# Kernel optimization log

Measured on AMD Instinct MI355X. Metric: run time of the kernel, lower is better.

## Reference

```python
import jax, jax.numpy as jnp
from jax import lax
import numpy as np

LRELU_SLOPE = 0.2
DEMOD_EPS = 1e-8


def _mod_conv(x, style, weight, bias, demodulate, pad):
    """StyleGAN2 modulated conv via grouped conv (groups = batch).
    x: [B,Cin,H,W]; style: [B,Cin]; weight: [Cout,Cin,kh,kw]; bias: [Cout]."""
    B, Cin, H, W = x.shape
    Cout, _, kh, kw = weight.shape
    # per-sample modulated weight [B,Cout,Cin,kh,kw]
    wt = weight[None] * style[:, None, :, None, None]
    if demodulate:
        wt = wt / jnp.sqrt(jnp.sum(wt ** 2, axis=(2, 3, 4), keepdims=True) + DEMOD_EPS)
    out = lax.conv_general_dilated(
        x.reshape(1, B * Cin, H, W),
        wt.reshape(B * Cout, Cin, kh, kw),
        window_strides=(1, 1),
        padding=[(pad, pad), (pad, pad)],
        dimension_numbers=('NCHW', 'OIHW', 'NCHW'),
        feature_group_count=B,
    )
    return out.reshape(B, Cout, H, W) + bias[None, :, None, None]


def setup_inputs() -> dict:
    key = jax.random.key(0)
    ks = jax.random.split(key, 16)
    B, Cin, Cout, Wd, H = 4, 512, 256, 512, 64
    f32 = jnp.float32
    d = {
        'x': jax.random.normal(ks[0], (B, Cin, H, H), f32),
        'w': jax.random.normal(ks[1], (B, Wd), f32),
        # conv1: Cin->Cout 3x3
        'w1': jax.random.normal(ks[2], (Cout, Cin, 3, 3), f32) / np.float32(np.sqrt(Cin * 9)),
        'b1': jax.random.normal(ks[3], (Cout,), f32) * 0.01,
        'a1w': jax.random.normal(ks[4], (Cin, Wd), f32) / np.float32(np.sqrt(Wd)),
        'a1b': jnp.ones((Cin,), f32),
        # conv2: Cout->Cout 3x3
        'w2': jax.random.normal(ks[5], (Cout, Cout, 3, 3), f32) / np.float32(np.sqrt(Cout * 9)),
        'b2': jax.random.normal(ks[6], (Cout,), f32) * 0.01,
        'a2w': jax.random.normal(ks[7], (Cout, Wd), f32) / np.float32(np.sqrt(Wd)),
        'a2b': jnp.ones((Cout,), f32),
        # to_rgb: Cout->3 1x1, no demodulation
        'w3': jax.random.normal(ks[8], (3, Cout, 1, 1), f32) / np.float32(np.sqrt(Cout)),
        'b3': jax.random.normal(ks[9], (3,), f32) * 0.01,
        'a3w': jax.random.normal(ks[10], (Cout, Wd), f32) / np.float32(np.sqrt(Wd)),
        'a3b': jnp.ones((Cout,), f32),
    }
    return d


def reference(x, w, w1, b1, a1w, a1b, w2, b2, a2w, a2b, w3, b3, a3w, a3b):
    B, C, H, W = x.shape
    # nn.Upsample(scale_factor=2, mode='bilinear', align_corners=False) == half-pixel bilinear
    xu = jax.image.resize(x, (B, C, 2 * H, 2 * W), method='bilinear')
    s1 = w @ a1w.T + a1b                      # affine -> per-sample style [B,Cin]
    h = jax.nn.leaky_relu(_mod_conv(xu, s1, w1, b1, True, 1), LRELU_SLOPE)
    s2 = w @ a2w.T + a2b
    h = jax.nn.leaky_relu(_mod_conv(h, s2, w2, b2, True, 1), LRELU_SLOPE)
    s3 = w @ a3w.T + a3b
    rgb = jax.nn.leaky_relu(_mod_conv(h, s3, w3, b3, False, 0), LRELU_SLOPE)
    return (h, rgb)
```

## Files before the change

### kernel.cpp

```cpp
#include <hip/hip_runtime.h>
#include <stdint.h>

typedef __attribute__((ext_vector_type(8))) short bhalf8;
typedef __attribute__((ext_vector_type(4))) float fx4;

__device__ __forceinline__ unsigned short f2bf(float f) {
    unsigned u = __builtin_bit_cast(unsigned, f);
    unsigned r = (u + 0x7fffu + ((u >> 16) & 1u)) >> 16;
    return (unsigned short)r;
}
__device__ __forceinline__ float bf2f(unsigned short h) {
    unsigned u = ((unsigned)h) << 16;
    return __builtin_bit_cast(float, u);
}
__device__ __forceinline__ float lrelu(float v) { return v > 0.f ? v : 0.2f * v; }

typedef __attribute__((address_space(1))) void as1_void;
typedef __attribute__((address_space(3))) void as3_void;
__device__ __forceinline__ void gl_lds16(const void* g, void* l) {
    __builtin_amdgcn_global_load_lds((as1_void*)(void*)g, (as3_void*)l, 16, 0, 0);
}

__global__ __launch_bounds__(256) void prep_kernel(
    const float* __restrict__ w1, const float* __restrict__ w2,
    unsigned short* __restrict__ wp1, unsigned short* __restrict__ wp2,
    const float* __restrict__ w,
    const float* __restrict__ a1w, const float* __restrict__ a1b,
    const float* __restrict__ a2w, const float* __restrict__ a2b,
    const float* __restrict__ a3w, const float* __restrict__ a3b,
    float* __restrict__ s1, float* __restrict__ s2, float* __restrict__ s3,
    float* __restrict__ rgbpart)
{
    const int bid = blockIdx.x;
    const int t = threadIdx.x;
    if (bid < 6912) {
        int tid = bid * 256 + t;
        const int N1 = 1179648, N2 = 589824;
        if (tid < N1) {
            int e = tid & 7, m = (tid >> 3) & 127, kh = (tid >> 10) & 3;
            int dx = (tid >> 12) % 3, ic = (tid / 12288) & 15;
            int dy = (tid / 196608) % 3, mblk = tid / 589824;
            int o = mblk * 128 + m, ci = ic * 32 + kh * 8 + e;
            wp1[tid] = f2bf(w1[((size_t)o * 512 + ci) * 9 + dy * 3 + dx]);
        } else if (tid < N1 + N2) {
            int t2 = tid - N1;
            int e = t2 & 7, m = (t2 >> 3) & 127, kh = (t2 >> 10) & 3;
            int dx = (t2 >> 12) % 3, ic = (t2 / 12288) & 7;
            int dy = (t2 / 98304) % 3, mblk = t2 / 294912;
            int o = mblk * 128 + m, ci = ic * 32 + kh * 8 + e;
            wp2[t2] = f2bf(w2[((size_t)o * 256 + ci) * 9 + dy * 3 + dx]);
        }
    } else if (bid < 7936) {
        int gw = (bid - 6912) * 4 + (t >> 6);
        int lane = t & 63;
        int b = gw >> 10, r = gw & 1023;
        const float* arow; const float* abias; float* dst;
        if (r < 512)      { arow = a1w + (size_t)r * 512;        abias = a1b + r;       dst = s1 + b * 512 + r; }
        else if (r < 768) { int rr = r - 512; arow = a2w + (size_t)rr * 512; abias = a2b + rr; dst = s2 + b * 256 + rr; }
        else              { int rr = r - 768; arow = a3w + (size_t)rr * 512; abias = a3b + rr; dst = s3 + b * 256 + rr; }
        const float* wrow = w + b * 512;
        float acc = 0.f;
        #pragma unroll
        for (int j = 0; j < 8; ++j) {
            int c = lane + j * 64;
            acc += wrow[c] * arow[c];
        }
        #pragma unroll
        for (int off = 32; off; off >>= 1) acc += __shfl_down(acc, off, 64);
        if (lane == 0) *dst = acc + *abias;
    } else {
        int i = (bid - 7936) * 256 + t;
        rgbpart[i] = 0.f;
    }
}

__global__ __launch_bounds__(256) void us_demod_kernel(
    const float* __restrict__ x, const float* __restrict__ s1,
    unsigned short* __restrict__ xu,
    const float* __restrict__ w1, const float* __restrict__ w2,
    const float* __restrict__ s2,
    float* __restrict__ d1, float* __restrict__ d2)
{
    const int bidg = blockIdx.x;
    const int t = threadIdx.x;
    if (bidg < 2048) {
        __shared__ float Lt[3][64][68];
        const int bid = bidg;
        const int cch = bid & 7, k = (bid >> 3) & 63, b = bid >> 9;
        const int c0 = cch * 64;
        {
            const int px4 = t & 15, cc4 = t >> 4;
            #pragma unroll
            for (int r = 0; r < 3; ++r) {
                int sy = k - 1 + r; sy = sy < 0 ? 0 : (sy > 63 ? 63 : sy);
                float4 v[4];
                #pragma unroll
                for (int j = 0; j < 4; ++j)
                    v[j] = *(const float4*)&x[((size_t)(b * 512 + c0 + cc4 * 4 + j) * 64 + sy) * 64 + px4 * 4];
                #pragma unroll
                for (int o = 0; o < 4; ++o) {
                    fx4 w4;
                    w4[0] = ((const float*)&v[0])[o];
                    w4[1] = ((const float*)&v[1])[o];
                    w4[2] = ((const float*)&v[2])[o];
                    w4[3] = ((const float*)&v[3])[o];
                    *(fx4*)&Lt[r][px4 * 4 + o][cc4 * 4] = w4;
                }
            }
        }
        __syncthreads();

        const int oct = t & 7, xob = t >> 3;
        float sty[8];
        #pragma unroll
        for (int j = 0; j < 8; ++j) sty[j] = s1[b * 512 + c0 + oct * 8 + j];

        #pragma unroll
        for (int half = 0; half < 2; ++half) {
            const int yo = 2 * k + half;
            const int rA = half ? 1 : 0, rB = rA + 1;
            const float wyA = half ? 0.75f : 0.25f, wyB = half ? 0.25f : 0.75f;
            #pragma unroll
            for (int i = 0; i < 4; ++i) {
                const int xo = xob + i * 32;
                const int kk = xo >> 1;
                int sx0, sx1; float wx0, wx1;
                if ((xo & 1) == 0) { sx0 = kk > 0 ? kk - 1 : 0; sx1 = kk; wx0 = 0.25f; wx1 = 0.75f; }
                else               { sx0 = kk; sx1 = kk < 63 ? kk + 1 : 63; wx0 = 0.75f; wx1 = 0.25f; }
                unsigned pk[4];
                #pragma unroll
                for (int h = 0; h < 2; ++h) {
                    const fx4 a0 = *(const fx4*)&Lt[rA][sx0][oct * 8 + h * 4];
                    const fx4 a1 = *(const fx4*)&Lt[rA][sx1][oct * 8 + h * 4];
                    const fx4 b0 = *(const fx4*)&Lt[rB][sx0][oct * 8 + h * 4];
                    const fx4 b1 = *(const fx4*)&Lt[rB][sx1][oct * 8 + h * 4];
                    #pragma unroll
                    for (int j2 = 0; j2 < 2; ++j2) {
                        float v0 = wyA * (wx0 * a0[j2 * 2]     + wx1 * a1[j2 * 2])
                                 + wyB * (wx0 * b0[j2 * 2]     + wx1 * b1[j2 * 2]);
                        float v1 = wyA * (wx0 * a0[j2 * 2 + 1] + wx1 * a1[j2 * 2 + 1])
                                 + wyB * (wx0 * b0[j2 * 2 + 1] + wx1 * b1[j2 * 2 + 1]);
                        v0 *= sty[h * 4 + j2 * 2];
                        v1 *= sty[h * 4 + j2 * 2 + 1];
                        pk[h * 2 + j2] = (unsigned)f2bf(v0) | ((unsigned)f2bf(v1) << 16);
                    }
                }
                *(int4*)&xu[((size_t)(b * 128 + yo) * 128 + xo) * 512 + c0 + oct * 8] =
                    make_int4(pk[0], pk[1], pk[2], pk[3]);
            }
        }
    } else {
        __shared__ float sv[512];
        __shared__ float red[4];
        int blk = bidg - 2048;
        int conv = blk >> 10, b = (blk >> 8) & 3, o = blk & 255;
        int cin = conv ? 256 : 512;
        const float* s = conv ? (s2 + b * 256) : (s1 + b * 512);
        const float* row = (conv ? w2 : w1) + (size_t)o * cin * 9;
        for (int i = t; i < cin; i += 256) { float v = s[i]; sv[i] = v * v; }
        __syncthreads();
        float sum = 0.f;
        int n = cin * 9;
        for (int k = t; k < n; k += 256) {
            float v = row[k];
            sum += v * v * sv[k / 9];
        }
        #pragma unroll
        for (int off = 32; off; off >>= 1) sum += __shfl_down(sum, off, 64);
        if ((t & 63) == 0) red[t >> 6] = sum;
        __syncthreads();
        if (t == 0) {
            float tot = red[0] + red[1] + red[2] + red[3];
            (conv ? d2 : d1)[b * 256 + o] = rsqrtf(tot + 1e-8f);
        }
    }
}

template<int CIN, bool IS_CONV2>
__global__ __launch_bounds__(512, 4) void conv3x3_kernel(
    const unsigned short* __restrict__ inp,
    const unsigned short* __restrict__ wpack,
    const float* __restrict__ dvec,
    const float* __restrict__ bias,
    const float* __restrict__ post,
    unsigned short* __restrict__ outmod,
    float* __restrict__ outf,
    const float* __restrict__ w3,
    float* __restrict__ rgbpart)
{
    constexpr int NIC = CIN / 32;
    __shared__ __attribute__((aligned(16))) short Alds[2][12288];
    __shared__ __attribute__((aligned(16))) short Blds[4][128][32];
    const int tid = threadIdx.x;
    const int lane = tid & 63;
    const int wvi = tid >> 6;
    const int bid = blockIdx.x;
    const int y0 = (bid & 63) << 1;
    const int mblk = (bid >> 6) & 1;
    const int b = bid >> 7;
    const int wm = (wvi >> 2) * 64;
    const int row = (wvi >> 1) & 1;
    const int wn = (wvi & 1) * 64;
    const int lhi = lane >> 4;
    const int llo = lane & 15;

    const int xg = tid >> 2, i8 = tid & 3;
    const int i8s = i8 ^ ((xg >> 1) & 3);

    fx4 acc[4][4];
    #pragma unroll
    for (int mt = 0; mt < 4; ++mt)
        #pragma unroll
        for (int nt = 0; nt < 4; ++nt) acc[mt][nt] = (fx4){0.f, 0.f, 0.f, 0.f};

    auto stageB = [&](int ic) {
        #pragma unroll
        for (int rr = 0; rr < 4; ++rr) {
            const int yy = y0 - 1 + rr;
            char* dstB = (char*)&Blds[rr][0][0] + tid * 16;
            if ((unsigned)yy < 128u) {
                gl_lds16(inp + ((size_t)(b * 128 + yy) * 128 + xg) * CIN + ic * 32 + i8s * 8, dstB);
            } else {
                *(int4*)dstB = make_int4(0, 0, 0, 0);
            }
        }
    };
    auto stageA = [&](int ic, int dy, int buf) {
        const unsigned short* asrc = wpack + ((size_t)(mblk * 3 + dy) * NIC + ic) * 12288;
        #pragma unroll
        for (int j = 0; j < 3; ++j) {
            int g = tid + j * 512;
            gl_lds16(asrc + (size_t)g * 8, (char*)&Alds[buf][0] + g * 16);
        }
    };

    stageB(0);
    stageA(0, 0, 0);
    __syncthreads();

    int par = 0;
    for (int ic = 0; ic < NIC; ++ic) {
        #pragma unroll
        for (int dy = 0; dy < 3; ++dy) {
            const bool last = (ic == NIC - 1) && (dy == 2);
            if (!last) {
                const int nic = (dy == 2) ? ic + 1 : ic;
                const int ndy = (dy == 2) ? 0 : dy + 1;
                stageA(nic, ndy, par ^ 1);
            }
            const short* Ab = &Alds[par][0];
            const short* Brow = &Blds[row + dy][0][0];
            #pragma unroll
            for (int dx = 0; dx < 3; ++dx) {
                bhalf8 af[4], bfr[4];
                #pragma unroll
                for (int mt = 0; mt < 4; ++mt)
                    af[mt] = *(const bhalf8*)&Ab[dx * 4096 + (lhi * 128 + wm + mt * 16 + llo) * 8];
                #pragma unroll
                for (int nt = 0; nt < 4; ++nt) {
                    const int s = wn + nt * 16 + llo + dx;
                    if ((nt == 0 && dx == 0) || (nt == 3 && dx == 2)) {
                        const bool edge = (s == 0) || (s == 129);
                        const int sp = edge ? 0 : (s - 1);
                        const int key = (sp >> 1) & 3;
                        bhalf8 v = *(const bhalf8*)&Brow[sp * 32 + ((lhi ^ key) << 3)];
                        bhalf8 z = {0, 0, 0, 0, 0, 0, 0, 0};
                        bfr[nt] = edge ? z : v;
                    } else {
                        const int sp = s - 1;
                        const int key = (sp >> 1) & 3;
                        bfr[nt] = *(const bhalf8*)&Brow[sp * 32 + ((lhi ^ key) << 3)];
                    }
                }
                __builtin_amdgcn_s_setprio(1);
                #pragma unroll
                for (int mt = 0; mt < 4; ++mt)
                    #pragma unroll
                    for (int nt = 0; nt < 4; ++nt)
                        acc[mt][nt] = __builtin_amdgcn_mfma_f32_16x16x32_bf16(
                            af[mt], bfr[nt], acc[mt][nt], 0, 0, 0);
                __builtin_amdgcn_s_setprio(0);
            }
            if (dy == 2 && ic + 1 < NIC) {
                __syncthreads();
                stageB(ic + 1);
            }
            if (!last) __syncthreads();
            par ^= 1;
        }
    }

    const int y = y0 + row;
    if constexpr (!IS_CONV2) {
        #pragma unroll
        for (int mt = 0; mt < 4; ++mt) {
            const int o0 = mblk * 128 + wm + mt * 16 + lhi * 4;
            const fx4 d4 = *(const fx4*)(dvec + b * 256 + o0);
            const fx4 bb4 = *(const fx4*)(bias + o0);
            const fx4 p4 = *(const fx4*)(post + b * 256 + o0);
            #pragma unroll
            for (int nt = 0; nt < 4; ++nt) {
                const int xo = wn + nt * 16 + llo;
                unsigned lo = 0, hi = 0;
                #pragma unroll
                for (int r = 0; r < 4; ++r) {
                    float v = acc[mt][nt][r] * d4[r] + bb4[r];
                    v = lrelu(v);
                    unsigned short ub = f2bf(v * p4[r]);
                    if (r < 2) lo |= (unsigned)ub << (16 * r);
                    else       hi |= (unsigned)ub << (16 * (r - 2));
                }
                *(uint2*)&outmod[((size_t)(b * 128 + y) * 128 + xo) * 256 + o0] = make_uint2(lo, hi);
            }
        }
    } else {
        #pragma unroll
        for (int nt = 0; nt < 4; ++nt) {
            const int xo = wn + nt * 16 + llo;
            float pq0 = 0.f, pq1 = 0.f, pq2 = 0.f;
            #pragma unroll
            for (int mt = 0; mt < 4; ++mt) {
                const int o0 = mblk * 128 + wm + mt * 16 + lhi * 4;
                const fx4 d4 = *(const fx4*)(dvec + b * 256 + o0);
                const fx4 bb4 = *(const fx4*)(bias + o0);
                const fx4 p4 = *(const fx4*)(post + b * 256 + o0);
                const fx4 wq0 = *(const fx4*)(w3 + o0);
                const fx4 wq1 = *(const fx4*)(w3 + 256 + o0);
                const fx4 wq2 = *(const fx4*)(w3 + 512 + o0);
                #pragma unroll
                for (int r = 0; r < 4; ++r) {
                    float v = acc[mt][nt][r] * d4[r] + bb4[r];
                    v = lrelu(v);
                    outf[(((size_t)b * 256 + o0 + r) * 128 + y) * 128 + xo] = v;
                    const float hv = v * p4[r];
                    pq0 += wq0[r] * hv;
                    pq1 += wq1[r] * hv;
                    pq2 += wq2[r] * hv;
                }
            }
            pq0 += __shfl_xor(pq0, 16, 64); pq0 += __shfl_xor(pq0, 32, 64);
            pq1 += __shfl_xor(pq1, 16, 64); pq1 += __shfl_xor(pq1, 32, 64);
            pq2 += __shfl_xor(pq2, 16, 64); pq2 += __shfl_xor(pq2, 32, 64);
            if (lhi == 0) {
                float* rp = rgbpart + (size_t)b * 49152 + (size_t)y * 128 + xo;
                atomicAdd(rp, pq0);
                atomicAdd(rp + 16384, pq1);
                atomicAdd(rp + 32768, pq2);
            }
        }
    }
}

__global__ __launch_bounds__(256) void rgb_finish_kernel(
    const float* __restrict__ part, const float* __restrict__ b3,
    float* __restrict__ out)
{
    int i = blockIdx.x * 256 + threadIdx.x;
    int q = (i >> 14) % 3;
    out[i] = lrelu(part[i] + b3[q]);
}

extern "C" void kernel_launch(void* const* d_in, const int* in_sizes, int n_in,
                              void* d_out, int out_size, void* d_ws, size_t ws_size,
                              hipStream_t stream) {
    const float* x   = (const float*)d_in[0];
    const float* w   = (const float*)d_in[1];
    const float* w1  = (const float*)d_in[2];
    const float* b1  = (const float*)d_in[3];
    const float* a1w = (const float*)d_in[4];
    const float* a1b = (const float*)d_in[5];
    const float* w2  = (const float*)d_in[6];
    const float* b2  = (const float*)d_in[7];
    const float* a2w = (const float*)d_in[8];
    const float* a2b = (const float*)d_in[9];
    const float* w3  = (const float*)d_in[10];
    const float* b3  = (const float*)d_in[11];
    const float* a3w = (const float*)d_in[12];
    const float* a3b = (const float*)d_in[13];

    char* ws = (char*)d_ws;
    unsigned short* xu  = (unsigned short*)(ws);
    unsigned short* t1  = (unsigned short*)(ws + 67108864);
    unsigned short* wp1 = (unsigned short*)(ws + 100663296);
    unsigned short* wp2 = (unsigned short*)(ws + 103022592);
    float* s1 = (float*)(ws + 104202240);
    float* s2 = (float*)(ws + 104210432);
    float* s3 = (float*)(ws + 104214528);
    float* d1 = (float*)(ws + 104218624);
    float* d2 = (float*)(ws + 104222720);
    float* rgbpart = (float*)(ws + 104226816);

    float* h_out   = (float*)d_out;
    float* rgb_out = h_out + 16777216;

    prep_kernel<<<8704, 256, 0, stream>>>(w1, w2, wp1, wp2,
                                          w, a1w, a1b, a2w, a2b, a3w, a3b,
                                          s1, s2, s3, rgbpart);
    us_demod_kernel<<<4096, 256, 0, stream>>>(x, s1, xu, w1, w2, s2, d1, d2);
    conv3x3_kernel<512, false><<<512, 512, 0, stream>>>(xu, wp1, d1, b1, s2, t1, nullptr, nullptr, nullptr);
    conv3x3_kernel<256, true><<<512, 512, 0, stream>>>(t1, wp2, d2, b2, s3, nullptr, h_out, w3, rgbpart);
    rgb_finish_kernel<<<768, 256, 0, stream>>>(rgbpart, b3, rgb_out);
}
```

Measured before the change: 353.5 us.

## Split B staging into halves overlapped with MMA and coalesce conv1 epilogue via LDS

The input-row staging is split into two halves that are prefetched alongside the weight tiles during earlier dy steps. This removes the extra barrier and the exposed B load at each input-channel boundary. The conv1 epilogue now writes bf16 results into a swizzled LDS buffer, reusing the shared memory as a single raw array, then stores them to global memory with fully coalesced row-contiguous writes. The cost is two extra barriers and an LDS round trip in the epilogue.

Result: slower. 450.6 us (+27.4%).

```diff
diff --git a/kernel.cpp b/kernel.cpp
--- a/kernel.cpp
+++ b/kernel.cpp
@@ -189,8 +189,9 @@
     float* __restrict__ rgbpart)
 {
     constexpr int NIC = CIN / 32;
-    __shared__ __attribute__((aligned(16))) short Alds[2][12288];
-    __shared__ __attribute__((aligned(16))) short Blds[4][128][32];
+    __shared__ __attribute__((aligned(16))) char SMEM[81920];
+    short (*Alds)[12288] = (short(*)[12288])SMEM;
+    short (*Blds)[128][32] = (short(*)[128][32])(SMEM + 49152);
     const int tid = threadIdx.x;
     const int lane = tid & 63;
     const int wvi = tid >> 6;
@@ -213,9 +214,9 @@
         #pragma unroll
         for (int nt = 0; nt < 4; ++nt) acc[mt][nt] = (fx4){0.f, 0.f, 0.f, 0.f};
 
-    auto stageB = [&](int ic) {
-        #pragma unroll
-        for (int rr = 0; rr < 4; ++rr) {
+    auto stageB2 = [&](int ic, int rp) {
+        #pragma unroll
+        for (int rr = rp * 2; rr < rp * 2 + 2; ++rr) {
             const int yy = y0 - 1 + rr;
             char* dstB = (char*)&Blds[rr][0][0] + tid * 16;
             if ((unsigned)yy < 128u) {
@@ -234,19 +235,24 @@
         }
     };
 
-    stageB(0);
+    stageB2(0, 0);
     stageA(0, 0, 0);
     __syncthreads();
 
     int par = 0;
     for (int ic = 0; ic < NIC; ++ic) {
+        const bool lastic = (ic == NIC - 1);
         #pragma unroll
         for (int dy = 0; dy < 3; ++dy) {
-            const bool last = (ic == NIC - 1) && (dy == 2);
-            if (!last) {
-                const int nic = (dy == 2) ? ic + 1 : ic;
-                const int ndy = (dy == 2) ? 0 : dy + 1;
-                stageA(nic, ndy, par ^ 1);
+            const bool last = lastic && (dy == 2);
+            if (dy == 0) {
+                stageA(ic, 1, par ^ 1);
+                stageB2(ic, 1);
+            } else if (dy == 1) {
+                stageA(ic, 2, par ^ 1);
+            } else if (!lastic) {
+                stageA(ic + 1, 0, par ^ 1);
+                stageB2(ic + 1, 0);
             }
             const short* Ab = &Alds[par][0];
             const short* Brow = &Blds[row + dy][0][0];
@@ -281,23 +287,21 @@
                             af[mt], bfr[nt], acc[mt][nt], 0, 0, 0);
                 __builtin_amdgcn_s_setprio(0);
             }
-            if (dy == 2 && ic + 1 < NIC) {
-                __syncthreads();
-                stageB(ic + 1);
-            }
             if (!last) __syncthreads();
             par ^= 1;
         }
     }
 
-    const int y = y0 + row;
     if constexpr (!IS_CONV2) {
+        __syncthreads();
+        uint2* L = (uint2*)SMEM;
         #pragma unroll
         for (int mt = 0; mt < 4; ++mt) {
             const int o0 = mblk * 128 + wm + mt * 16 + lhi * 4;
             const fx4 d4 = *(const fx4*)(dvec + b * 256 + o0);
             const fx4 bb4 = *(const fx4*)(bias + o0);
             const fx4 p4 = *(const fx4*)(post + b * 256 + o0);
+            const int slot = (wm >> 2) + mt * 4 + lhi;
             #pragma unroll
             for (int nt = 0; nt < 4; ++nt) {
                 const int xo = wn + nt * 16 + llo;
@@ -310,10 +314,21 @@
                     if (r < 2) lo |= (unsigned)ub << (16 * r);
                     else       hi |= (unsigned)ub << (16 * (r - 2));
                 }
-                *(uint2*)&outmod[((size_t)(b * 128 + y) * 128 + xo) * 256 + o0] = make_uint2(lo, hi);
-            }
+                L[((row << 7) + xo) * 32 + (slot ^ (xo & 31))] = make_uint2(lo, hi);
+            }
+        }
+        __syncthreads();
+        #pragma unroll
+        for (int p = 0; p < 16; ++p) {
+            const int i = p * 512 + tid;
+            const int pix = i >> 5;
+            const int slot = i & 31;
+            const uint2 v = L[pix * 32 + (slot ^ (pix & 31))];
+            const int yl = pix >> 7, xx = pix & 127;
+            *(uint2*)&outmod[((size_t)(b * 128 + y0 + yl) * 128 + xx) * 256 + mblk * 128 + slot * 4] = v;
         }
     } else {
+        const int y = y0 + row;
         #pragma unroll
         for (int nt = 0; nt < 4; ++nt) {
             const int xo = wn + nt * 16 + llo;
```
